# Optimization experiments

Hardware: AMD Instinct MI355X
Metric: run time of the kernel (lower is better)

Reference implementation:

```python
import jax, jax.numpy as jnp
import numpy as np

GAMMA0 = 1.0


def patch_to_image(patches):
    # patches: [b, n_patch, patch_dim, 1, T] -> image [b, 1, g*p, g*p, T]
    b, n_patch, patch_dim, _, T = patches.shape
    p = int(patch_dim ** 0.5)
    g = int(n_patch ** 0.5)
    img = patches[:, :, :, 0, :]                      # [b, n_patch, p*p, T]
    img = jnp.transpose(img, (0, 3, 1, 2))            # [b, T, n_patch, p*p]
    img = img.reshape(b, T, g, g, p, p)
    img = jnp.transpose(img, (0, 1, 2, 4, 3, 5)).reshape(b, T, 1, g * p, g * p)
    return jnp.transpose(img, (0, 2, 3, 4, 1))        # [b, 1, g*p, g*p, T]


def setup_inputs() -> dict:
    key = jax.random.key(0)
    k0, k1, k2, k3, k4, k5 = jax.random.split(key, 6)
    X = jax.random.normal(k0, (32, 64, 300, 1, 50), dtype=jnp.float32)
    U = jax.random.normal(k1, (32, 1, 40, 1, 50), dtype=jnp.float32)
    x0 = jax.random.normal(k2, (32, 64, 300, 1), dtype=jnp.float32)
    # dictionaries, column-normalized like torch's norm(dim=2, keepdim=True)
    A = jax.random.uniform(k3, (300, 300), dtype=jnp.float32)
    A = A / jnp.linalg.norm(A, axis=0, keepdims=True)
    B = jax.random.uniform(k4, (300, 40), dtype=jnp.float32)
    B = B / jnp.linalg.norm(B, axis=0, keepdims=True)
    C = jax.random.uniform(k5, (256, 300), dtype=jnp.float32)
    C = C / jnp.linalg.norm(C, axis=0, keepdims=True)
    return {"X": X, "U": U, "x0": x0, "A": A, "B": B, "C": C}


def reference(X, U, x0, A, B, C):
    # X: [b, P, 300, 1, T]  U: [b, 1, 40, 1, T]  x0: [b, P, 300, 1]
    # Prediction x_hat_t = A @ x_{t-1}, with x_{-1} = x0 (vectorized over T)
    x_prev = jnp.concatenate([x0[..., None], X[..., :-1]], axis=-1)   # [b,P,300,1,T]
    X_pred = jnp.einsum('ij,bpjut->bpiut', A, x_prev)                 # [b,P,300,1,T]
    # Reconstruction recon_t = C @ x_t, assembled into frames
    recon = jnp.einsum('dj,bpjut->bpdut', C, X)                       # [b,P,256,1,T]
    vid_recon = patch_to_image(recon)                                 # [b,1,128,128,T]
    # Cause state: gamma_t * sum_patches |x_t|
    Bu = jnp.einsum('ij,bqjut->bqiut', B, U)                          # [b,1,300,1,T]
    gamma = GAMMA0 * (1.0 + jnp.exp(-Bu)) / 2.0
    X_U = gamma * jnp.sum(jnp.abs(X), axis=1, keepdims=True)          # [b,1,300,1,T]
    return (vid_recon, X_pred, X_U)
```

## Files before the change

kernel.cpp:

```cpp
#include <hip/hip_runtime.h>

typedef float f32x4 __attribute__((ext_vector_type(4)));
typedef unsigned long long ull;

#define OFF_PRED 26214400
#define OFF_XU   56934400
#define NBP 8
#define LROW 328

__device__ inline unsigned pack4_fp8(float a, float b, float c, float d) {
    int r = __builtin_amdgcn_cvt_pk_fp8_f32(a, b, 0, false);
    r = __builtin_amdgcn_cvt_pk_fp8_f32(c, d, r, true);
    return (unsigned)r;
}

__global__ void build_M(const float* __restrict__ A, const float* __restrict__ C,
                        unsigned* __restrict__ M) {
    int idx = blockIdx.x * 256 + threadIdx.x;
    if (idx >= 51200) return;
    int d = idx * 4;
    int e0 = d & 7, lane = (d >> 3) & 63, fs = d >> 9;
    int mt = fs / 10, ks = fs % 10;
    int m = mt * 16 + (lane & 15);
    int k = ks * 32 + (lane >> 4) * 8 + e0;
    float f0 = 0.f, f1 = 0.f, f2 = 0.f, f3 = 0.f;
    const float* src = nullptr;
    if (m < 256) src = C + m * 300;
    else if (m < 556) src = A + (m - 256) * 300;
    if (src) {
        if (k + 0 < 300) f0 = src[k + 0];
        if (k + 1 < 300) f1 = src[k + 1];
        if (k + 2 < 300) f2 = src[k + 2];
        if (k + 3 < 300) f3 = src[k + 3];
    }
    M[idx] = pack4_fp8(f0, f1, f2, f3);
}

__global__ __launch_bounds__(512, 2) void gemm_main(
    const float* __restrict__ X, const float* __restrict__ x0,
    const char* __restrict__ M, float* __restrict__ out)
{
    __shared__ char ldsb[64 * LROW];
    const int tid = threadIdx.x;
    const int wave = tid >> 6, lane = tid & 63;
    const int lr = lane & 15, lg = lane >> 4;
    const int g = wave;
    const int bp0 = blockIdx.x * NBP;

    int offg[8], offl[8];
    #pragma unroll
    for (int u = 0; u < 8; u++) {
        int i = tid + u * 512;
        int t = i % 50, jq = i / 50;
        offg[u] = jq * 200 + t;
        offl[u] = (t + 1) * LROW + jq * 4;
    }
    const bool v7 = tid < 166;

    #pragma unroll
    for (int u = 0; u < 6; u++) {
        int i = tid + u * 512;
        if (i < 2624) ((ull*)ldsb)[i] = 0ULL;
    }

    long long mf[5][10];
    #pragma unroll
    for (int j = 0; j < 5; j++)
        #pragma unroll
        for (int ks = 0; ks < 10; ks++)
            mf[j][ks] = *(const long long*)(M + (((g * 5 + j) * 10 + ks) * 64 + lane) * 8);

    __syncthreads();

    for (int it = 0; it < NBP; ++it) {
        const int bp = bp0 + it;
        const int b = bp >> 6, p = bp & 63;
        const float* Xbp = X + bp * 15000;

        if (tid < 75) {
            f32x4 v = *(const f32x4*)(x0 + bp * 300 + tid * 4);
            *(unsigned*)(ldsb + tid * 4) = pack4_fp8(v.x, v.y, v.z, v.w);
        }
        #pragma unroll
        for (int u = 0; u < 8; u++) if (u < 7 || v7) {
            const float* s = Xbp + offg[u];
            *(unsigned*)(ldsb + offl[u]) = pack4_fp8(s[0], s[50], s[100], s[150]);
        }
        __syncthreads();

        f32x4 acc[5][4];
        #pragma unroll
        for (int j = 0; j < 5; j++)
            #pragma unroll
            for (int nt = 0; nt < 4; nt++)
                acc[j][nt] = (f32x4){0.f, 0.f, 0.f, 0.f};

        #pragma unroll
        for (int ks = 0; ks < 10; ks++) {
            long long a0 = *(const long long*)(ldsb + (0 * 16 + lr) * LROW + ks * 32 + lg * 8);
            long long a1 = *(const long long*)(ldsb + (1 * 16 + lr) * LROW + ks * 32 + lg * 8);
            long long a2 = *(const long long*)(ldsb + (2 * 16 + lr) * LROW + ks * 32 + lg * 8);
            long long a3 = *(const long long*)(ldsb + (3 * 16 + lr) * LROW + ks * 32 + lg * 8);
            #pragma unroll
            for (int j = 0; j < 5; j++) {
                acc[j][0] = __builtin_amdgcn_mfma_f32_16x16x32_fp8_fp8(a0, mf[j][ks], acc[j][0], 0, 0, 0);
                acc[j][1] = __builtin_amdgcn_mfma_f32_16x16x32_fp8_fp8(a1, mf[j][ks], acc[j][1], 0, 0, 0);
                acc[j][2] = __builtin_amdgcn_mfma_f32_16x16x32_fp8_fp8(a2, mf[j][ks], acc[j][2], 0, 0, 0);
                acc[j][3] = __builtin_amdgcn_mfma_f32_16x16x32_fp8_fp8(a3, mf[j][ks], acc[j][3], 0, 0, 0);
            }
        }

        {
            const int gr = p >> 3, gc = p & 7;
            #pragma unroll
            for (int j = 0; j < 5; j++) {
                int colm = g * 80 + j * 16 + lr;
                if (colm < 256) {
                    int base = b * 819200 + ((gr * 16 + (colm >> 4)) * 128 + gc * 16 + (colm & 15)) * 50;
                    #pragma unroll
                    for (int nt = 0; nt < 4; nt++) {
                        int t0 = nt * 16 + lg * 4;
                        if (t0 == 0) {
                            out[base + 0] = acc[j][0][1];
                            out[base + 1] = acc[j][0][2];
                            out[base + 2] = acc[j][0][3];
                        } else if (t0 <= 46) {
                            f32x4 v = acc[j][nt];
                            __builtin_memcpy(&out[base + t0 - 1], &v, 16);
                        } else if (t0 == 48) {
                            out[base + 47] = acc[j][nt][0];
                            out[base + 48] = acc[j][nt][1];
                            out[base + 49] = acc[j][nt][2];
                        }
                    }
                } else if (colm < 556) {
                    int base = OFF_PRED + (bp * 300 + (colm - 256)) * 50;
                    #pragma unroll
                    for (int nt = 0; nt < 4; nt++) {
                        int t0 = nt * 16 + lg * 4;
                        if (t0 <= 46) {
                            f32x4 v = acc[j][nt];
                            __builtin_memcpy(&out[base + t0], &v, 16);
                        } else if (t0 == 48) {
                            out[base + 48] = acc[j][nt][0];
                            out[base + 49] = acc[j][nt][1];
                        }
                    }
                }
            }
        }
        __syncthreads();
    }
}

__global__ void xu_kernel(const float* __restrict__ X, const float* __restrict__ U,
                          const float* __restrict__ B, float* __restrict__ out) {
    int id = blockIdx.x * 256 + threadIdx.x;
    if (id >= 480000) return;
    int t = id % 50;
    int i = (id / 50) % 300;
    int b = id / 15000;
    const float* xp = X + b * 960000 + i * 50 + t;
    float s = 0.f;
    #pragma unroll 8
    for (int pp = 0; pp < 64; pp++) s += fabsf(xp[pp * 15000]);
    float bu = 0.f;
    const float* up = U + b * 2000 + t;
    const float* Bp = B + i * 40;
    #pragma unroll 8
    for (int q = 0; q < 40; q++) bu += Bp[q] * up[q * 50];
    out[OFF_XU + id] = 0.5f * (1.f + expf(-bu)) * s;
}

extern "C" void kernel_launch(void* const* d_in, const int* in_sizes, int n_in,
                              void* d_out, int out_size, void* d_ws, size_t ws_size,
                              hipStream_t stream) {
    const float* X  = (const float*)d_in[0];
    const float* U  = (const float*)d_in[1];
    const float* x0 = (const float*)d_in[2];
    const float* A  = (const float*)d_in[3];
    const float* B  = (const float*)d_in[4];
    const float* C  = (const float*)d_in[5];
    float* out = (float*)d_out;
    unsigned* M = (unsigned*)d_ws;

    build_M<<<200, 256, 0, stream>>>(A, C, M);
    gemm_main<<<256, 512, 0, stream>>>(X, x0, (const char*)M, out);
    xu_kernel<<<1875, 256, 0, stream>>>(X, U, B, out);
}
```

Measured before the change: 144.4 us.

## Double-buffer LDS and prefetch next patch's X tile during MFMA and stores

Doubles the LDS staging buffer and software-pipelines the per-patch loop. The next patch's X and x0 values are loaded into registers in two halves, one issued before the MFMA loop and one before the output stores, then packed into the alternate buffer. This overlaps global load latency with compute and the store epilogue and removes one barrier per iteration. In exchange it raises register and LDS use, which may reduce occupancy under launch_bounds(512,2).

After: 213.5 us. 47.8% more time.

```diff
diff --git a/kernel.cpp b/kernel.cpp
--- a/kernel.cpp
+++ b/kernel.cpp
@@ -7,6 +7,7 @@
 #define OFF_XU   56934400
 #define NBP 8
 #define LROW 328
+#define BUFSZ (64 * LROW)
 
 __device__ inline unsigned pack4_fp8(float a, float b, float c, float d) {
     int r = __builtin_amdgcn_cvt_pk_fp8_f32(a, b, 0, false);
@@ -40,7 +41,7 @@
     const float* __restrict__ X, const float* __restrict__ x0,
     const char* __restrict__ M, float* __restrict__ out)
 {
-    __shared__ char ldsb[64 * LROW];
+    __shared__ char ldsb[2 * BUFSZ];
     const int tid = threadIdx.x;
     const int wave = tid >> 6, lane = tid & 63;
     const int lr = lane & 15, lg = lane >> 4;
@@ -58,9 +59,9 @@
     const bool v7 = tid < 166;
 
     #pragma unroll
-    for (int u = 0; u < 6; u++) {
+    for (int u = 0; u < 11; u++) {
         int i = tid + u * 512;
-        if (i < 2624) ((ull*)ldsb)[i] = 0ULL;
+        if (i < 2 * BUFSZ / 8) ((ull*)ldsb)[i] = 0ULL;
     }
 
     long long mf[5][10];
@@ -70,23 +71,47 @@
         for (int ks = 0; ks < 10; ks++)
             mf[j][ks] = *(const long long*)(M + (((g * 5 + j) * 10 + ks) * 64 + lane) * 8);
 
+    float sxa[4][4], sxb[4][4], s0x[4];
+
+#define LOAD_A(bp_) { const float* Xb_ = X + (bp_) * 15000;                          \
+    _Pragma("unroll")                                                                 \
+    for (int u = 0; u < 4; u++) {                                                     \
+        const float* s_ = Xb_ + offg[u];                                              \
+        sxa[u][0] = s_[0]; sxa[u][1] = s_[50]; sxa[u][2] = s_[100]; sxa[u][3] = s_[150]; \
+    }                                                                                 \
+    if (tid < 75) { f32x4 v_ = *(const f32x4*)(x0 + (bp_) * 300 + tid * 4);           \
+        s0x[0] = v_.x; s0x[1] = v_.y; s0x[2] = v_.z; s0x[3] = v_.w; } }
+
+#define LOAD_B(bp_) { const float* Xb_ = X + (bp_) * 15000;                          \
+    _Pragma("unroll")                                                                 \
+    for (int u = 4; u < 8; u++) if (u < 7 || v7) {                                    \
+        const float* s_ = Xb_ + offg[u];                                              \
+        sxb[u-4][0] = s_[0]; sxb[u-4][1] = s_[50]; sxb[u-4][2] = s_[100]; sxb[u-4][3] = s_[150]; \
+    } }
+
+#define WRITE_A(wb_) {                                                                \
+    _Pragma("unroll")                                                                 \
+    for (int u = 0; u < 4; u++)                                                       \
+        *(unsigned*)((wb_) + offl[u]) = pack4_fp8(sxa[u][0], sxa[u][1], sxa[u][2], sxa[u][3]); \
+    if (tid < 75) *(unsigned*)((wb_) + tid * 4) = pack4_fp8(s0x[0], s0x[1], s0x[2], s0x[3]); }
+
+#define WRITE_B(wb_) {                                                                \
+    _Pragma("unroll")                                                                 \
+    for (int u = 4; u < 8; u++) if (u < 7 || v7)                                      \
+        *(unsigned*)((wb_) + offl[u]) = pack4_fp8(sxb[u-4][0], sxb[u-4][1], sxb[u-4][2], sxb[u-4][3]); }
+
+    LOAD_A(bp0); LOAD_B(bp0);
+    WRITE_A(ldsb); WRITE_B(ldsb);
     __syncthreads();
 
+    #pragma unroll 1
     for (int it = 0; it < NBP; ++it) {
         const int bp = bp0 + it;
         const int b = bp >> 6, p = bp & 63;
-        const float* Xbp = X + bp * 15000;
-
-        if (tid < 75) {
-            f32x4 v = *(const f32x4*)(x0 + bp * 300 + tid * 4);
-            *(unsigned*)(ldsb + tid * 4) = pack4_fp8(v.x, v.y, v.z, v.w);
-        }
-        #pragma unroll
-        for (int u = 0; u < 8; u++) if (u < 7 || v7) {
-            const float* s = Xbp + offg[u];
-            *(unsigned*)(ldsb + offl[u]) = pack4_fp8(s[0], s[50], s[100], s[150]);
-        }
-        __syncthreads();
+        char* rb = ldsb + (it & 1) * BUFSZ;
+        char* wb = ldsb + ((it & 1) ^ 1) * BUFSZ;
+
+        if (it + 1 < NBP) LOAD_A(bp + 1);
 
         f32x4 acc[5][4];
         #pragma unroll
@@ -97,10 +122,10 @@
 
         #pragma unroll
         for (int ks = 0; ks < 10; ks++) {
-            long long a0 = *(const long long*)(ldsb + (0 * 16 + lr) * LROW + ks * 32 + lg * 8);
-            long long a1 = *(const long long*)(ldsb + (1 * 16 + lr) * LROW + ks * 32 + lg * 8);
-            long long a2 = *(const long long*)(ldsb + (2 * 16 + lr) * LROW + ks * 32 + lg * 8);
-            long long a3 = *(const long long*)(ldsb + (3 * 16 + lr) * LROW + ks * 32 + lg * 8);
+            long long a0 = *(const long long*)(rb + (0 * 16 + lr) * LROW + ks * 32 + lg * 8);
+            long long a1 = *(const long long*)(rb + (1 * 16 + lr) * LROW + ks * 32 + lg * 8);
+            long long a2 = *(const long long*)(rb + (2 * 16 + lr) * LROW + ks * 32 + lg * 8);
+            long long a3 = *(const long long*)(rb + (3 * 16 + lr) * LROW + ks * 32 + lg * 8);
             #pragma unroll
             for (int j = 0; j < 5; j++) {
                 acc[j][0] = __builtin_amdgcn_mfma_f32_16x16x32_fp8_fp8(a0, mf[j][ks], acc[j][0], 0, 0, 0);
@@ -109,6 +134,8 @@
                 acc[j][3] = __builtin_amdgcn_mfma_f32_16x16x32_fp8_fp8(a3, mf[j][ks], acc[j][3], 0, 0, 0);
             }
         }
+
+        if (it + 1 < NBP) { WRITE_A(wb); LOAD_B(bp + 1); }
 
         {
             const int gr = p >> 3, gc = p & 7;
@@ -149,6 +176,8 @@
                 }
             }
         }
+
+        if (it + 1 < NBP) WRITE_B(wb);
         __syncthreads();
     }
 }
```

## Split GEMM into one block per patch and output half, swizzle block order

Applied to the files above, without the earlier changes.

Replaces the persistent 256-block kernel, which looped over 8 batch-patches per block, with 4096 blocks of 256 threads. Each block handles one batch-patch and one half of the 640 output columns. Block indices are remapped so neighbouring blocks share patches, and only the padding regions of LDS are zeroed. This aims to raise occupancy and parallelism across the MI355X compute units. In exchange, each patch's X tile is loaded and converted to FP8 twice, and the M fragments are reloaded per block instead of being amortised over several patches.

Measured after the change: 153.8 us. +6.5%, slower.

```diff
diff --git a/kernel.cpp b/kernel.cpp
--- a/kernel.cpp
+++ b/kernel.cpp
@@ -5,7 +5,6 @@
 
 #define OFF_PRED 26214400
 #define OFF_XU   56934400
-#define NBP 8
 #define LROW 328
 
 __device__ inline unsigned pack4_fp8(float a, float b, float c, float d) {
@@ -36,120 +35,122 @@
     M[idx] = pack4_fp8(f0, f1, f2, f3);
 }
 
-__global__ __launch_bounds__(512, 2) void gemm_main(
+__global__ __launch_bounds__(256, 2) void gemm_main(
     const float* __restrict__ X, const float* __restrict__ x0,
     const char* __restrict__ M, float* __restrict__ out)
 {
     __shared__ char ldsb[64 * LROW];
     const int tid = threadIdx.x;
+    const int orig = ((blockIdx.x & 7) << 9) + (blockIdx.x >> 3);
+    const int bp = orig >> 1, mhalf = orig & 1;
+    const int b = bp >> 6, p = bp & 63;
+    const float* Xbp = X + bp * 15000;
+
     const int wave = tid >> 6, lane = tid & 63;
     const int lr = lane & 15, lg = lane >> 4;
     const int g = wave;
-    const int bp0 = blockIdx.x * NBP;
-
-    int offg[8], offl[8];
-    #pragma unroll
-    for (int u = 0; u < 8; u++) {
-        int i = tid + u * 512;
-        int t = i % 50, jq = i / 50;
-        offg[u] = jq * 200 + t;
-        offl[u] = (t + 1) * LROW + jq * 4;
-    }
-    const bool v7 = tid < 166;
-
-    #pragma unroll
-    for (int u = 0; u < 6; u++) {
-        int i = tid + u * 512;
-        if (i < 2624) ((ull*)ldsb)[i] = 0ULL;
-    }
 
     long long mf[5][10];
     #pragma unroll
     for (int j = 0; j < 5; j++)
         #pragma unroll
         for (int ks = 0; ks < 10; ks++)
-            mf[j][ks] = *(const long long*)(M + (((g * 5 + j) * 10 + ks) * 64 + lane) * 8);
+            mf[j][ks] = *(const long long*)(M +
+                ((((mhalf * 20 + g * 5 + j) * 10 + ks) * 64 + lane) * 8));
 
+    if (tid < 256) {
+        int i = tid;
+        if (i < 357) {
+            int row = i / 7, c = i % 7;
+            *(unsigned*)(ldsb + row * LROW + 300 + c * 4) = 0u;
+        }
+        int i2 = tid + 101;
+    }
+    if (tid < 101) {
+        int i = tid + 256;
+        int row = i / 7, c = i % 7;
+        *(unsigned*)(ldsb + row * LROW + 300 + c * 4) = 0u;
+    }
+    #pragma unroll
+    for (int u = 0; u < 3; u++) {
+        int i = tid + u * 256;
+        if (i < 533) *(ull*)(ldsb + 51 * LROW + i * 8) = 0ULL;
+    }
+
+    if (tid < 75) {
+        f32x4 v = *(const f32x4*)(x0 + bp * 300 + tid * 4);
+        *(unsigned*)(ldsb + tid * 4) = pack4_fp8(v.x, v.y, v.z, v.w);
+    }
+    #pragma unroll
+    for (int u = 0; u < 15; u++) {
+        int i = tid + u * 256;
+        if (i < 3750) {
+            int t = i % 50, jq = i / 50;
+            const float* s = Xbp + jq * 200 + t;
+            *(unsigned*)(ldsb + (t + 1) * LROW + jq * 4) =
+                pack4_fp8(s[0], s[50], s[100], s[150]);
+        }
+    }
     __syncthreads();
 
-    for (int it = 0; it < NBP; ++it) {
-        const int bp = bp0 + it;
-        const int b = bp >> 6, p = bp & 63;
-        const float* Xbp = X + bp * 15000;
+    f32x4 acc[5][4];
+    #pragma unroll
+    for (int j = 0; j < 5; j++)
+        #pragma unroll
+        for (int nt = 0; nt < 4; nt++)
+            acc[j][nt] = (f32x4){0.f, 0.f, 0.f, 0.f};
 
-        if (tid < 75) {
-            f32x4 v = *(const f32x4*)(x0 + bp * 300 + tid * 4);
-            *(unsigned*)(ldsb + tid * 4) = pack4_fp8(v.x, v.y, v.z, v.w);
+    #pragma unroll
+    for (int ks = 0; ks < 10; ks++) {
+        long long a0 = *(const long long*)(ldsb + (0 * 16 + lr) * LROW + ks * 32 + lg * 8);
+        long long a1 = *(const long long*)(ldsb + (1 * 16 + lr) * LROW + ks * 32 + lg * 8);
+        long long a2 = *(const long long*)(ldsb + (2 * 16 + lr) * LROW + ks * 32 + lg * 8);
+        long long a3 = *(const long long*)(ldsb + (3 * 16 + lr) * LROW + ks * 32 + lg * 8);
+        #pragma unroll
+        for (int j = 0; j < 5; j++) {
+            acc[j][0] = __builtin_amdgcn_mfma_f32_16x16x32_fp8_fp8(a0, mf[j][ks], acc[j][0], 0, 0, 0);
+            acc[j][1] = __builtin_amdgcn_mfma_f32_16x16x32_fp8_fp8(a1, mf[j][ks], acc[j][1], 0, 0, 0);
+            acc[j][2] = __builtin_amdgcn_mfma_f32_16x16x32_fp8_fp8(a2, mf[j][ks], acc[j][2], 0, 0, 0);
+            acc[j][3] = __builtin_amdgcn_mfma_f32_16x16x32_fp8_fp8(a3, mf[j][ks], acc[j][3], 0, 0, 0);
         }
-        #pragma unroll
-        for (int u = 0; u < 8; u++) if (u < 7 || v7) {
-            const float* s = Xbp + offg[u];
-            *(unsigned*)(ldsb + offl[u]) = pack4_fp8(s[0], s[50], s[100], s[150]);
-        }
-        __syncthreads();
+    }
 
-        f32x4 acc[5][4];
-        #pragma unroll
-        for (int j = 0; j < 5; j++)
+    const int gr = p >> 3, gc = p & 7;
+    #pragma unroll
+    for (int j = 0; j < 5; j++) {
+        int colm = mhalf * 320 + g * 80 + j * 16 + lr;
+        if (colm < 256) {
+            int base = b * 819200 + ((gr * 16 + (colm >> 4)) * 128 + gc * 16 + (colm & 15)) * 50;
             #pragma unroll
-            for (int nt = 0; nt < 4; nt++)
-                acc[j][nt] = (f32x4){0.f, 0.f, 0.f, 0.f};
-
-        #pragma unroll
-        for (int ks = 0; ks < 10; ks++) {
-            long long a0 = *(const long long*)(ldsb + (0 * 16 + lr) * LROW + ks * 32 + lg * 8);
-            long long a1 = *(const long long*)(ldsb + (1 * 16 + lr) * LROW + ks * 32 + lg * 8);
-            long long a2 = *(const long long*)(ldsb + (2 * 16 + lr) * LROW + ks * 32 + lg * 8);
-            long long a3 = *(const long long*)(ldsb + (3 * 16 + lr) * LROW + ks * 32 + lg * 8);
+            for (int nt = 0; nt < 4; nt++) {
+                int t0 = nt * 16 + lg * 4;
+                if (t0 == 0) {
+                    out[base + 0] = acc[j][0][1];
+                    out[base + 1] = acc[j][0][2];
+                    out[base + 2] = acc[j][0][3];
+                } else if (t0 <= 46) {
+                    f32x4 v = acc[j][nt];
+                    __builtin_memcpy(&out[base + t0 - 1], &v, 16);
+                } else if (t0 == 48) {
+                    out[base + 47] = acc[j][nt][0];
+                    out[base + 48] = acc[j][nt][1];
+                    out[base + 49] = acc[j][nt][2];
+                }
+            }
+        } else if (colm < 556) {
+            int base = OFF_PRED + (bp * 300 + (colm - 256)) * 50;
             #pragma unroll
-            for (int j = 0; j < 5; j++) {
-                acc[j][0] = __builtin_amdgcn_mfma_f32_16x16x32_fp8_fp8(a0, mf[j][ks], acc[j][0], 0, 0, 0);
-                acc[j][1] = __builtin_amdgcn_mfma_f32_16x16x32_fp8_fp8(a1, mf[j][ks], acc[j][1], 0, 0, 0);
-                acc[j][2] = __builtin_amdgcn_mfma_f32_16x16x32_fp8_fp8(a2, mf[j][ks], acc[j][2], 0, 0, 0);
-                acc[j][3] = __builtin_amdgcn_mfma_f32_16x16x32_fp8_fp8(a3, mf[j][ks], acc[j][3], 0, 0, 0);
-            }
-        }
-
-        {
-            const int gr = p >> 3, gc = p & 7;
-            #pragma unroll
-            for (int j = 0; j < 5; j++) {
-                int colm = g * 80 + j * 16 + lr;
-                if (colm < 256) {
-                    int base = b * 819200 + ((gr * 16 + (colm >> 4)) * 128 + gc * 16 + (colm & 15)) * 50;
-                    #pragma unroll
-                    for (int nt = 0; nt < 4; nt++) {
-                        int t0 = nt * 16 + lg * 4;
-                        if (t0 == 0) {
-                            out[base + 0] = acc[j][0][1];
-                            out[base + 1] = acc[j][0][2];
-                            out[base + 2] = acc[j][0][3];
-                        } else if (t0 <= 46) {
-                            f32x4 v = acc[j][nt];
-                            __builtin_memcpy(&out[base + t0 - 1], &v, 16);
-                        } else if (t0 == 48) {
-                            out[base + 47] = acc[j][nt][0];
-                            out[base + 48] = acc[j][nt][1];
-                            out[base + 49] = acc[j][nt][2];
-                        }
-                    }
-                } else if (colm < 556) {
-                    int base = OFF_PRED + (bp * 300 + (colm - 256)) * 50;
-                    #pragma unroll
-                    for (int nt = 0; nt < 4; nt++) {
-                        int t0 = nt * 16 + lg * 4;
-                        if (t0 <= 46) {
-                            f32x4 v = acc[j][nt];
-                            __builtin_memcpy(&out[base + t0], &v, 16);
-                        } else if (t0 == 48) {
-                            out[base + 48] = acc[j][nt][0];
-                            out[base + 49] = acc[j][nt][1];
-                        }
-                    }
+            for (int nt = 0; nt < 4; nt++) {
+                int t0 = nt * 16 + lg * 4;
+                if (t0 <= 46) {
+                    f32x4 v = acc[j][nt];
+                    __builtin_memcpy(&out[base + t0], &v, 16);
+                } else if (t0 == 48) {
+                    out[base + 48] = acc[j][nt][0];
+                    out[base + 49] = acc[j][nt][1];
                 }
             }
         }
-        __syncthreads();
     }
 }
 
@@ -185,6 +186,6 @@
     unsigned* M = (unsigned*)d_ws;
 
     build_M<<<200, 256, 0, stream>>>(A, C, M);
-    gemm_main<<<256, 512, 0, stream>>>(X, x0, (const char*)M, out);
+    gemm_main<<<4096, 256, 0, stream>>>(X, x0, (const char*)M, out);
     xu_kernel<<<1875, 256, 0, stream>>>(X, U, B, out);
 }
```
